# Optimization experiments

Hardware: AMD Instinct MI355X
Metric: run time of the kernel (lower is better)

The kernel has to match this reference:

```python
import jax, jax.numpy as jnp
import numpy as np

OBS_DIM, ACT_DIM, HID_DIM, FEAT = 256, 32, 1024, 512
T_STEPS, BATCH = 64, 512
LOG2PI = float(np.log(2.0 * np.pi))


def _mlp(h, w0, b0, w1, b1, w2, b2):
    # 2 hidden elu layers + linear head (MLPDecoder mean; fix_std Normal, std=1)
    x = jax.nn.elu(h @ w0.T + b0)
    x = jax.nn.elu(x @ w1.T + b1)
    return x @ w2.T + b2


def _gru(x, h, w_ih, w_hh, b_ih, b_hh):
    # torch.nn.GRUCell semantics
    gi = x @ w_ih.T + b_ih
    gh = h @ w_hh.T + b_hh
    i_r, i_z, i_n = jnp.split(gi, 3, axis=-1)
    h_r, h_z, h_n = jnp.split(gh, 3, axis=-1)
    r = jax.nn.sigmoid(i_r + h_r)
    z = jax.nn.sigmoid(i_z + h_z)
    n = jnp.tanh(i_n + r * h_n)
    return (1.0 - z) * n + z * h


def setup_inputs() -> dict:
    key = jax.random.key(0)
    ks = jax.random.split(key, 20)
    d = {}
    d['obs'] = jax.random.normal(ks[0], (T_STEPS, BATCH, OBS_DIM), jnp.float32)
    d['action'] = jax.random.normal(ks[1], (T_STEPS, BATCH, ACT_DIM), jnp.float32)
    d['reward'] = jax.random.normal(ks[2], (T_STEPS, BATCH, 1), jnp.float32)
    in_dim = OBS_DIM + ACT_DIM
    s = lambda fan_in: 1.0 / np.sqrt(fan_in)
    d['gru_w_ih'] = jax.random.normal(ks[3], (3 * HID_DIM, in_dim), jnp.float32) * s(in_dim)
    d['gru_w_hh'] = jax.random.normal(ks[4], (3 * HID_DIM, HID_DIM), jnp.float32) * s(HID_DIM)
    d['gru_b_ih'] = jnp.zeros((3 * HID_DIM,), jnp.float32)
    d['gru_b_hh'] = jnp.zeros((3 * HID_DIM,), jnp.float32)
    for name, out_dim, base in (('obs', OBS_DIM, 5), ('rew', 1, 11)):
        d[f'{name}_w0'] = jax.random.normal(ks[base], (FEAT, HID_DIM), jnp.float32) * s(HID_DIM)
        d[f'{name}_b0'] = jnp.zeros((FEAT,), jnp.float32)
        d[f'{name}_w1'] = jax.random.normal(ks[base + 1], (FEAT, FEAT), jnp.float32) * s(FEAT)
        d[f'{name}_b1'] = jnp.zeros((FEAT,), jnp.float32)
        d[f'{name}_w2'] = jax.random.normal(ks[base + 2], (out_dim, FEAT), jnp.float32) * s(FEAT)
        d[f'{name}_b2'] = jnp.zeros((out_dim,), jnp.float32)
    return d


def reference(obs, action, reward,
              gru_w_ih, gru_w_hh, gru_b_ih, gru_b_hh,
              obs_w0, obs_b0, obs_w1, obs_b1, obs_w2, obs_b2,
              rew_w0, rew_b0, rew_w1, rew_b1, rew_w2, rew_b2):
    T, B = obs.shape[0], obs.shape[1]

    def normal_logprob_sum(x, mean):
        # Normal(mean, std=1): -0.5*(x-mean)^2 - 0.5*log(2*pi), summed
        return -0.5 * jnp.sum((x - mean) ** 2 + LOG2PI)

    h0 = _gru(jnp.concatenate([obs[0], jnp.zeros_like(action[0])], axis=1),
              jnp.zeros((B, HID_DIM), obs.dtype),
              gru_w_ih, gru_w_hh, gru_b_ih, gru_b_hh)

    def step(h, xs):
        obs_t, act_t, rew_t = xs
        obs_mean = _mlp(h, obs_w0, obs_b0, obs_w1, obs_b1, obs_w2, obs_b2)
        lp_obs = normal_logprob_sum(obs_t, obs_mean)
        rew_mean = _mlp(h, rew_w0, rew_b0, rew_w1, rew_b1, rew_w2, rew_b2)
        lp_rew = normal_logprob_sum(rew_t, rew_mean)
        # feed predicted obs (mode) + ground-truth action back into the GRU
        x = jnp.concatenate([obs_mean, act_t], axis=1)
        h_next = _gru(x, h, gru_w_ih, gru_w_hh, gru_b_ih, gru_b_hh)
        return h_next, (obs_mean, rew_mean, lp_obs, lp_rew)

    _, (pre_obs, pre_reward, lp_obs, lp_rew) = jax.lax.scan(
        step, h0, (obs, action, reward))

    denom = jnp.asarray(T * B, obs.dtype)
    pre_obs_loss = -jnp.sum(lp_obs) / denom
    pre_reward_loss = -jnp.sum(lp_rew) / denom
    loss = pre_obs_loss + pre_reward_loss  # action_mimic=False -> action loss is 0
    return loss, pre_obs, pre_reward
```

## Files before the change

### kernel.cpp

```cpp
#include <hip/hip_runtime.h>
#include <stdint.h>

#define T_STEPS 64
#define BATCH   512
#define OBS_DIM 256
#define ACT_DIM 32
#define HID     1024
#define FEAT    512
#define GDIM    3072
#define KIH     288
#define NBLK    256
#define GMEMB   32
#define LOG2PI  1.8378770664093453f
#define HWREG_XCC_ID 14356

typedef __attribute__((ext_vector_type(8))) short  short8;
typedef __attribute__((ext_vector_type(4))) float  floatx4;
typedef __attribute__((ext_vector_type(4))) unsigned int uintx4;
typedef unsigned long long ull;

__device__ __forceinline__ float bf2f(unsigned int u) {
    return __uint_as_float(u << 16);
}
__device__ __forceinline__ unsigned int f2bf(float f) {
    unsigned int u = __float_as_uint(f);
    return (u + 0x7FFFu + ((u >> 16) & 1u)) >> 16;
}
__device__ __forceinline__ float elu1(float x)  { return x > 0.f ? x : expm1f(x); }
__device__ __forceinline__ float sigm(float x)  { return 1.f / (1.f + expf(-x)); }

__device__ __forceinline__ unsigned int dev_ld(const unsigned int* p) {
    return __hip_atomic_load(p, __ATOMIC_RELAXED, __HIP_MEMORY_SCOPE_AGENT);
}
__device__ __forceinline__ ull dev_ld64(const ull* p) {
    return __hip_atomic_load(p, __ATOMIC_RELAXED, __HIP_MEMORY_SCOPE_AGENT);
}
__device__ __forceinline__ void dev_st(unsigned int* p, unsigned int v) {
    __hip_atomic_store(p, v, __ATOMIC_RELAXED, __HIP_MEMORY_SCOPE_AGENT);
}
__device__ __forceinline__ float dev_ldf(const float* p) {
    return __uint_as_float(dev_ld((const unsigned int*)p));
}

template<bool COH>
__device__ __forceinline__ unsigned int a_ld(const unsigned int* p) {
    return COH ? dev_ld(p) : *p;
}
template<bool COH>
__device__ __forceinline__ ull a_ld64(const ull* p) {
    return COH ? dev_ld64(p) : *p;
}
template<bool COH>
__device__ __forceinline__ void a_st(unsigned int* p, unsigned int v) {
    if (COH) dev_st(p, v); else *p = v;
}

struct ParamsReal {
    const float* obs; const float* action; const float* reward;
    const float* b_ih; const float* b_hh;
    const float* b1o; const float* b1r; const float* b2o; const float* b2r;
    const unsigned short* Ws1; const unsigned short* Wih;
    const unsigned short* W1o; const unsigned short* W1r;
    const unsigned short* W2o; const unsigned short* w2r;
    const float* bias_s1;
    unsigned short* Z1[2]; unsigned short* Z2[2]; unsigned short* Xbuf[2];
    unsigned short* hbf[2]; unsigned short* GHb[2]; float* h[2];
    float* accum; float* out;
    int* bar;
};
#define P ParamsReal

__device__ __forceinline__ void bar_fast() {
    asm volatile("" ::: "memory");
    __builtin_amdgcn_s_barrier();
    asm volatile("" ::: "memory");
}
__device__ __forceinline__ void bar_lds() {
    asm volatile("s_waitcnt lgkmcnt(0)" ::: "memory");
    __builtin_amdgcn_s_barrier();
    asm volatile("" ::: "memory");
}

__device__ __forceinline__ void gbar(int* cnt, int* gen, int& epoch, int members) {
    __syncthreads();
    if (threadIdx.x == 0) {
        __builtin_amdgcn_fence(__ATOMIC_RELEASE, "workgroup");
        epoch++;
        int prev = __hip_atomic_fetch_add(cnt, 1, __ATOMIC_RELAXED,
                                          __HIP_MEMORY_SCOPE_AGENT);
        if (prev == members * epoch - 1) {
            __hip_atomic_store(gen, epoch, __ATOMIC_RELAXED,
                               __HIP_MEMORY_SCOPE_AGENT);
        } else {
            while (__hip_atomic_load(gen, __ATOMIC_RELAXED,
                                     __HIP_MEMORY_SCOPE_AGENT) < epoch)
                __builtin_amdgcn_s_sleep(2);
        }
        __builtin_amdgcn_fence(__ATOMIC_ACQUIRE, "workgroup");
    }
    __syncthreads();
}

template<bool COH>
__device__ __forceinline__ void s1_stage(const P& p, unsigned short* lds,
                                         int g, int m,
                                         const unsigned short* hbf_r,
                                         unsigned short* Z1_w,
                                         unsigned short* GHb_w) {
    const int tid = threadIdx.x, lane = tid & 63, wv = tid >> 6;
    const int wr = wv & 1, wc = wv >> 1, fr = lane & 15, fq = lane >> 4;
    const int rowg = g * 64, col0 = m * 128;
    unsigned short* ldsA = lds;
    unsigned short* ldsB = lds + 64 * 136;

    floatx4 acc[2][4];
    floatx4 z4 = {0.f, 0.f, 0.f, 0.f};
#pragma unroll
    for (int mi = 0; mi < 2; ++mi)
#pragma unroll
        for (int n = 0; n < 4; ++n) acc[mi][n] = z4;

    const ull* Aq = (const ull*)(hbf_r + (size_t)rowg * HID);
    const unsigned short* Bg = p.Ws1 + (size_t)col0 * HID;

    ull apf[8];
#pragma unroll
    for (int j = 0; j < 8; ++j) { int f = tid + 256 * j;
        apf[j] = a_ld64<COH>(Aq + (size_t)(f >> 5) * 256 + (f & 31)); }
    uintx4 rb0[4], rb1[4];
#pragma unroll
    for (int i = 0; i < 4; ++i) { int c = tid + 256 * i;
        const unsigned short* bp = Bg + (size_t)(c >> 3) * HID + ((c & 7) << 3);
        rb0[i] = __builtin_nontemporal_load((const uintx4*)bp);
        rb1[i] = __builtin_nontemporal_load((const uintx4*)(bp + 64)); }

#define S1_MFMA(ASUB)                                                          \
    {                                                                          \
        _Pragma("unroll")                                                      \
        for (int ks = 0; ks < 2; ++ks) {                                       \
            short8 af[2], bf8[4];                                              \
            _Pragma("unroll")                                                  \
            for (int mi = 0; mi < 2; ++mi)                                     \
                af[mi] = *(const short8*)(ldsA + (wr * 32 + mi * 16 + fr) * 136 + (ASUB) + ks * 32 + fq * 8); \
            _Pragma("unroll")                                                  \
            for (int n = 0; n < 4; ++n)                                        \
                bf8[n] = *(const short8*)(ldsB + (wc * 64 + n * 16 + fr) * 72 + ks * 32 + fq * 8); \
            _Pragma("unroll")                                                  \
            for (int mi = 0; mi < 2; ++mi)                                     \
                _Pragma("unroll")                                              \
                for (int n = 0; n < 4; ++n)                                    \
                    acc[mi][n] = __builtin_amdgcn_mfma_f32_16x16x32_bf16(      \
                        af[mi], bf8[n], acc[mi][n], 0, 0, 0);                  \
        }                                                                      \
    }

    for (int it2 = 0; it2 < 8; ++it2) {
        bar_fast();
#pragma unroll
        for (int j = 0; j < 8; ++j) { int f = tid + 256 * j;
            *(ull*)(ldsA + (size_t)(f >> 5) * 136 + ((f & 31) << 2)) = apf[j]; }
#pragma unroll
        for (int i = 0; i < 4; ++i) { int c = tid + 256 * i;
            *(uintx4*)(ldsB + (c >> 3) * 72 + ((c & 7) << 3)) = rb0[i]; }
        bar_lds();
        if (it2 < 7) {
            int c2 = it2 + 1;
#pragma unroll
            for (int j = 0; j < 8; ++j) { int f = tid + 256 * j;
                apf[j] = a_ld64<COH>(Aq + (size_t)(f >> 5) * 256 + c2 * 32 + (f & 31)); }
            int k0n = (2 * it2 + 2) * 64;
#pragma unroll
            for (int i = 0; i < 4; ++i) { int c = tid + 256 * i;
                rb0[i] = __builtin_nontemporal_load((const uintx4*)
                    (Bg + (size_t)(c >> 3) * HID + k0n + ((c & 7) << 3))); }
        }
        S1_MFMA(0);
        bar_fast();
#pragma unroll
        for (int i = 0; i < 4; ++i) { int c = tid + 256 * i;
            *(uintx4*)(ldsB + (c >> 3) * 72 + ((c & 7) << 3)) = rb1[i]; }
        bar_lds();
        if (it2 < 7) {
            int k0n = (2 * it2 + 3) * 64;
#pragma unroll
            for (int i = 0; i < 4; ++i) { int c = tid + 256 * i;
                rb1[i] = __builtin_nontemporal_load((const uintx4*)
                    (Bg + (size_t)(c >> 3) * HID + k0n + ((c & 7) << 3))); }
        }
        S1_MFMA(64);
    }
#undef S1_MFMA

    const bool isZ1 = (col0 < 1024);
#pragma unroll
    for (int mi = 0; mi < 2; ++mi)
#pragma unroll
        for (int n = 0; n < 4; ++n)
#pragma unroll
            for (int j = 0; j < 4; ++j) {
                int row = rowg + wr * 32 + mi * 16 + fq * 4 + j;
                int col = col0 + wc * 64 + n * 16 + fr;
                float v = acc[mi][n][j] + p.bias_s1[col];
                unsigned int ow = f2bf(isZ1 ? elu1(v) : v);
                unsigned int pr = __shfl_xor(ow, 1, 64);
                if (!(fr & 1)) {
                    unsigned int pk = ow | (pr << 16);
                    if (isZ1)
                        a_st<COH>((unsigned int*)(Z1_w + row * HID + col), pk);
                    else
                        a_st<COH>((unsigned int*)GHb_w + (size_t)row * 1536 + ((col - 1024) >> 1), pk);
                }
            }
}

template<bool COH>
__device__ __forceinline__ void s2_stage(const P& p, unsigned short* lds,
                                         int g, int m,
                                         const unsigned short* Z1_r,
                                         unsigned short* Z2_w) {
    const int tid = threadIdx.x, lane = tid & 63, wv = tid >> 6;
    const int wr = wv & 1, wc = wv >> 1, fr = lane & 15, fq = lane >> 4;
    const int rowg = g * 64;
    const int z = m >> 4, col0 = (m & 15) * 32;
    unsigned short* ldsA = lds;
    unsigned short* ldsB = lds + 64 * 136;

    floatx4 acc[2];
    floatx4 z4 = {0.f, 0.f, 0.f, 0.f};
    acc[0] = z4; acc[1] = z4;

    const ull* Aq = (const ull*)(Z1_r + (size_t)rowg * HID + z * FEAT);
    const unsigned short* Bg = (z ? p.W1r : p.W1o) + (size_t)col0 * FEAT;
    const float* bias = z ? p.b1r : p.b1o;

    ull apf[8];
#pragma unroll
    for (int j = 0; j < 8; ++j) { int f = tid + 256 * j;
        apf[j] = a_ld64<COH>(Aq + (size_t)(f >> 5) * 256 + (f & 31)); }
    const unsigned short* bp0 = Bg + (size_t)(tid >> 3) * FEAT + ((tid & 7) << 3);
    uintx4 rb0 = *(const uintx4*)(bp0);
    uintx4 rb1 = *(const uintx4*)(bp0 + 64);

#define S2_MFMA(ASUB)                                                          \
    {                                                                          \
        _Pragma("unroll")                                                      \
        for (int ks = 0; ks < 2; ++ks) {                                       \
            short8 bf8 = *(const short8*)(ldsB + (wc * 16 + fr) * 72 + ks * 32 + fq * 8); \
            _Pragma("unroll")                                                  \
            for (int mi = 0; mi < 2; ++mi) {                                   \
                short8 af = *(const short8*)(ldsA + (wr * 32 + mi * 16 + fr) * 136 + (ASUB) + ks * 32 + fq * 8); \
                acc[mi] = __builtin_amdgcn_mfma_f32_16x16x32_bf16(af, bf8, acc[mi], 0, 0, 0); \
            }                                                                  \
        }                                                                      \
    }

    for (int it2 = 0; it2 < 4; ++it2) {
        bar_fast();
#pragma unroll
        for (int j = 0; j < 8; ++j) { int f = tid + 256 * j;
            *(ull*)(ldsA + (size_t)(f >> 5) * 136 + ((f & 31) << 2)) = apf[j]; }
        *(uintx4*)(ldsB + (tid >> 3) * 72 + ((tid & 7) << 3)) = rb0;
        bar_lds();
        if (it2 < 3) {
            int c2 = it2 + 1;
#pragma unroll
            for (int j = 0; j < 8; ++j) { int f = tid + 256 * j;
                apf[j] = a_ld64<COH>(Aq + (size_t)(f >> 5) * 256 + c2 * 32 + (f & 31)); }
            rb0 = *(const uintx4*)(bp0 + (2 * it2 + 2) * 64);
        }
        S2_MFMA(0);
        bar_fast();
        *(uintx4*)(ldsB + (tid >> 3) * 72 + ((tid & 7) << 3)) = rb1;
        bar_lds();
        if (it2 < 3) rb1 = *(const uintx4*)(bp0 + (2 * it2 + 3) * 64);
        S2_MFMA(64);
    }
#undef S2_MFMA

#pragma unroll
    for (int mi = 0; mi < 2; ++mi)
#pragma unroll
        for (int j = 0; j < 4; ++j) {
            int row = rowg + wr * 32 + mi * 16 + fq * 4 + j;
            int col = col0 + wc * 16 + fr;
            float v = acc[mi][j] + bias[col];
            unsigned int ow = f2bf(elu1(v));
            unsigned int pr = __shfl_xor(ow, 1, 64);
            if (!(fr & 1))
                a_st<COH>((unsigned int*)(Z2_w + row * HID + z * FEAT + col), ow | (pr << 16));
        }
}

template<bool COH>
__device__ __forceinline__ void s3_stage(const P& p, unsigned short* lds,
                                         int g, int m, int t,
                                         const unsigned short* Z2_r,
                                         unsigned short* Xbuf_w) {
    const int tid = threadIdx.x, lane = tid & 63, wv = tid >> 6;
    const int wr = wv & 1, wc = wv >> 1, fr = lane & 15, fq = lane >> 4;
    const int rowg = g * 64;

    if (m < 8) {
        const int col0 = m * 32;
        unsigned short* ldsA = lds;
        unsigned short* ldsB = lds + 64 * 136;
        floatx4 acc[2];
        floatx4 z4 = {0.f, 0.f, 0.f, 0.f};
        acc[0] = z4; acc[1] = z4;

        const ull* Aq = (const ull*)(Z2_r + (size_t)rowg * HID);
        const unsigned short* Bg = p.W2o + (size_t)col0 * FEAT;

        ull apf[8];
#pragma unroll
        for (int j = 0; j < 8; ++j) { int f = tid + 256 * j;
            apf[j] = a_ld64<COH>(Aq + (size_t)(f >> 5) * 256 + (f & 31)); }
        const unsigned short* bp0 = Bg + (size_t)(tid >> 3) * FEAT + ((tid & 7) << 3);
        uintx4 rb0 = *(const uintx4*)(bp0);
        uintx4 rb1 = *(const uintx4*)(bp0 + 64);

#define S3_MFMA(ASUB)                                                          \
        {                                                                      \
            _Pragma("unroll")                                                  \
            for (int ks = 0; ks < 2; ++ks) {                                   \
                short8 bf8 = *(const short8*)(ldsB + (wc * 16 + fr) * 72 + ks * 32 + fq * 8); \
                _Pragma("unroll")                                              \
                for (int mi = 0; mi < 2; ++mi) {                               \
                    short8 af = *(const short8*)(ldsA + (wr * 32 + mi * 16 + fr) * 136 + (ASUB) + ks * 32 + fq * 8); \
                    acc[mi] = __builtin_amdgcn_mfma_f32_16x16x32_bf16(af, bf8, acc[mi], 0, 0, 0); \
                }                                                              \
            }                                                                  \
        }

        for (int it2 = 0; it2 < 4; ++it2) {
            bar_fast();
#pragma unroll
            for (int j = 0; j < 8; ++j) { int f = tid + 256 * j;
                *(ull*)(ldsA + (size_t)(f >> 5) * 136 + ((f & 31) << 2)) = apf[j]; }
            *(uintx4*)(ldsB + (tid >> 3) * 72 + ((tid & 7) << 3)) = rb0;
            bar_lds();
            if (it2 < 3) {
                int c2 = it2 + 1;
#pragma unroll
                for (int j = 0; j < 8; ++j) { int f = tid + 256 * j;
                    apf[j] = a_ld64<COH>(Aq + (size_t)(f >> 5) * 256 + c2 * 32 + (f & 31)); }
                rb0 = *(const uintx4*)(bp0 + (2 * it2 + 2) * 64);
            }
            S3_MFMA(0);
            bar_fast();
            *(uintx4*)(ldsB + (tid >> 3) * 72 + ((tid & 7) << 3)) = rb1;
            bar_lds();
            if (it2 < 3) rb1 = *(const uintx4*)(bp0 + (2 * it2 + 3) * 64);
            S3_MFMA(64);
        }
#undef S3_MFMA

        const int col = col0 + wc * 16 + fr;
        const float b2oc = p.b2o[col];
        float lsum = 0.f;
#pragma unroll
        for (int mi = 0; mi < 2; ++mi)
#pragma unroll
            for (int j = 0; j < 4; ++j) {
                int row = rowg + wr * 32 + mi * 16 + fq * 4 + j;
                float mval = acc[mi][j] + b2oc;
                size_t oidx = (size_t)t * BATCH * OBS_DIM + (size_t)row * OBS_DIM + col;
                __builtin_nontemporal_store(mval, p.out + 1 + oidx);
                unsigned int ow = f2bf(mval);
                unsigned int pr = __shfl_xor(ow, 1, 64);
                if (!(fr & 1))
                    a_st<COH>((unsigned int*)(Xbuf_w + row * KIH + col), ow | (pr << 16));
                float d = __builtin_nontemporal_load(p.obs + oidx) - mval;
                lsum += d * d;
            }
#pragma unroll
        for (int off = 32; off > 0; off >>= 1) lsum += __shfl_down(lsum, off, 64);
        if (lane == 0) atomicAdd(p.accum + 0, lsum);
    } else if (m == 8) {
        for (int e = tid; e < 64 * 16; e += 256) {
            int row = rowg + (e >> 4), cp = (e & 15) * 2;
            const float* ap = p.action + ((size_t)t * BATCH + row) * ACT_DIM + cp;
            unsigned int lo = f2bf(__builtin_nontemporal_load(ap));
            unsigned int hi = f2bf(__builtin_nontemporal_load(ap + 1));
            a_st<COH>((unsigned int*)(Xbuf_w + row * KIH + OBS_DIM + cp), lo | (hi << 16));
        }
    } else if (m >= 16) {
        const int row = rowg + (m - 16) * 4 + wv;
        const ull* zq = (const ull*)(Z2_r + (size_t)row * HID + FEAT) + lane * 2;
        ull z0 = a_ld64<COH>(zq);
        ull z1 = a_ld64<COH>(zq + 1);
        short8 w8 = *(const short8*)(p.w2r + lane * 8);
        float s = 0.f;
#pragma unroll
        for (int k = 0; k < 4; ++k) {
            unsigned int u = (unsigned int)(z0 >> (16 * k)) & 0xFFFFu;
            s += bf2f(u) * bf2f((unsigned int)(unsigned short)w8[k]);
        }
#pragma unroll
        for (int k = 0; k < 4; ++k) {
            unsigned int u = (unsigned int)(z1 >> (16 * k)) & 0xFFFFu;
            s += bf2f(u) * bf2f((unsigned int)(unsigned short)w8[4 + k]);
        }
#pragma unroll
        for (int off = 32; off > 0; off >>= 1) s += __shfl_down(s, off, 64);
        if (lane == 0) {
            float mm = s + p.b2r[0];
            __builtin_nontemporal_store(
                mm, p.out + 1 + (size_t)T_STEPS * BATCH * OBS_DIM + (size_t)t * BATCH + row);
            float d = __builtin_nontemporal_load(p.reward + (size_t)t * BATCH + row) - mm;
            atomicAdd(p.accum + 1, d * d);
        }
    }
}

template<bool COH>
__device__ __forceinline__ void s4_stage(const P& p, unsigned short* lds,
                                         int g, int m, int use_gh,
                                         const unsigned short* Xbuf_r,
                                         const unsigned short* GHb_r,
                                         const float* h_r,
                                         float* h_w, unsigned short* hbf_w) {
    const int tid = threadIdx.x, lane = tid & 63, wv = tid >> 6;
    const int wr = wv & 1, wc = wv >> 1, fr = lane & 15, fq = lane >> 4;
    const int rowg = g * 64;
    const int col0 = m * 32;
    unsigned short* ldsA = lds;
    unsigned short* ldsB = lds + 64 * 104;

    floatx4 acc[3][2];
    floatx4 z4 = {0.f, 0.f, 0.f, 0.f};
#pragma unroll
    for (int g3 = 0; g3 < 3; ++g3) { acc[g3][0] = z4; acc[g3][1] = z4; }

    const ull* Xq = (const ull*)(Xbuf_r + (size_t)rowg * KIH);
    ull apf[6];
#pragma unroll
    for (int j = 0; j < 6; ++j) { int f = tid + 256 * j;
        apf[j] = a_ld64<COH>(Xq + (size_t)(f / 24) * 72 + (f % 24)); }

    uintx4 wpfA[5], wpfB[5];
#pragma unroll
    for (int j = 0; j < 5; ++j) { int f = tid + 256 * j;
        if (f < 1152) { int r = f / 12, ko = (f - r * 12) * 8;
            const unsigned short* wp =
                p.Wih + (size_t)((r >> 5) * HID + col0 + (r & 31)) * KIH + ko;
            wpfA[j] = __builtin_nontemporal_load((const uintx4*)wp);
            wpfB[j] = __builtin_nontemporal_load((const uintx4*)(wp + 96)); } }

#pragma unroll
    for (int c = 0; c < 3; ++c) {
        bar_fast();
#pragma unroll
        for (int j = 0; j < 6; ++j) { int f = tid + 256 * j;
            *(ull*)(ldsA + (size_t)(f / 24) * 104 + ((f % 24) << 2)) = apf[j]; }
#pragma unroll
        for (int j = 0; j < 5; ++j) { int f = tid + 256 * j;
            if (f < 1152) { int r = f / 12, ko = (f - r * 12) * 8;
                *(uintx4*)(ldsB + r * 104 + ko) = (c & 1) ? wpfB[j] : wpfA[j]; } }
        bar_lds();
        if (c < 2) {
#pragma unroll
            for (int j = 0; j < 6; ++j) { int f = tid + 256 * j;
                apf[j] = a_ld64<COH>(Xq + (size_t)(f / 24) * 72 + (c + 1) * 24 + (f % 24)); }
        }
        if (c == 0) {
#pragma unroll
            for (int j = 0; j < 5; ++j) { int f = tid + 256 * j;
                if (f < 1152) { int r = f / 12, ko = (f - r * 12) * 8;
                    wpfA[j] = __builtin_nontemporal_load((const uintx4*)
                        (p.Wih + (size_t)((r >> 5) * HID + col0 + (r & 31)) * KIH + 192 + ko)); } }
        }
#pragma unroll
        for (int ks = 0; ks < 3; ++ks) {
            short8 af[2];
#pragma unroll
            for (int mi = 0; mi < 2; ++mi)
                af[mi] = *(const short8*)(ldsA + (wr * 32 + mi * 16 + fr) * 104 + ks * 32 + fq * 8);
#pragma unroll
            for (int g3 = 0; g3 < 3; ++g3) {
                short8 bf8 = *(const short8*)(ldsB + (g3 * 32 + wc * 16 + fr) * 104 + ks * 32 + fq * 8);
#pragma unroll
                for (int mi = 0; mi < 2; ++mi)
                    acc[g3][mi] = __builtin_amdgcn_mfma_f32_16x16x32_bf16(
                        af[mi], bf8, acc[g3][mi], 0, 0, 0);
            }
        }
    }

    const int col = col0 + wc * 16 + fr;
    const float bir = p.b_ih[col];
    const float biz = p.b_ih[HID + col];
    const float bin = p.b_ih[2 * HID + col];
    float hrv[2][4], hzv[2][4], hnv[2][4], hpv[2][4];
    if (use_gh) {
        const unsigned int* GW = (const unsigned int*)GHb_r;
        const int cw = col >> 1, hi = col & 1;
#pragma unroll
        for (int mi = 0; mi < 2; ++mi)
#pragma unroll
            for (int j = 0; j < 4; ++j) {
                int row = rowg + wr * 32 + mi * 16 + fq * 4 + j;
                unsigned int ur = a_ld<COH>(GW + (size_t)row * 1536 + cw);
                unsigned int uz = a_ld<COH>(GW + (size_t)row * 1536 + 512 + cw);
                unsigned int un = a_ld<COH>(GW + (size_t)row * 1536 + 1024 + cw);
                hrv[mi][j] = bf2f(hi ? (ur >> 16) : (ur & 0xFFFFu));
                hzv[mi][j] = bf2f(hi ? (uz >> 16) : (uz & 0xFFFFu));
                hnv[mi][j] = bf2f(hi ? (un >> 16) : (un & 0xFFFFu));
                hpv[mi][j] = __uint_as_float(a_ld<COH>((const unsigned int*)(h_r + (size_t)row * HID + col)));
            }
    } else {
        float br = p.b_hh[col], bz = p.b_hh[HID + col], bn = p.b_hh[2 * HID + col];
#pragma unroll
        for (int mi = 0; mi < 2; ++mi)
#pragma unroll
            for (int j = 0; j < 4; ++j) {
                hrv[mi][j] = br; hzv[mi][j] = bz; hnv[mi][j] = bn; hpv[mi][j] = 0.f;
            }
    }
#pragma unroll
    for (int mi = 0; mi < 2; ++mi)
#pragma unroll
        for (int j = 0; j < 4; ++j) {
            int row = rowg + wr * 32 + mi * 16 + fq * 4 + j;
            float r  = sigm(acc[0][mi][j] + bir + hrv[mi][j]);
            float z  = sigm(acc[1][mi][j] + biz + hzv[mi][j]);
            float nn = tanhf(acc[2][mi][j] + bin + r * hnv[mi][j]);
            float hv = (1.f - z) * nn + z * hpv[mi][j];
            a_st<COH>((unsigned int*)(h_w + (size_t)row * HID + col), __float_as_uint(hv));
            unsigned int ow = f2bf(hv);
            unsigned int pr = __shfl_xor(ow, 1, 64);
            if (!(fr & 1))
                a_st<COH>((unsigned int*)(hbf_w + row * HID + col), ow | (pr << 16));
        }
}

template<bool COH>
__device__ void rollout(const P& p, unsigned short* lds, int g, int m) {
    int* gcnt = p.bar + g * 128;
    int* ggen = p.bar + g * 128 + 64;
    int epoch = 0;

    s4_stage<COH>(p, lds, g, m, 0, p.Xbuf[1], p.GHb[0], p.h[0], p.h[0], p.hbf[0]);
    gbar(gcnt, ggen, epoch, GMEMB);

    for (int t = 0; t < T_STEPS; ++t) {
        const int pr = t & 1, nx = (t + 1) & 1;
        s1_stage<COH>(p, lds, g, m, p.hbf[pr], p.Z1[pr], p.GHb[pr]);
        gbar(gcnt, ggen, epoch, GMEMB);
        s2_stage<COH>(p, lds, g, m, p.Z1[pr], p.Z2[pr]);
        gbar(gcnt, ggen, epoch, GMEMB);
        s3_stage<COH>(p, lds, g, m, t, p.Z2[pr], p.Xbuf[pr]);
        gbar(gcnt, ggen, epoch, GMEMB);
        if (t < T_STEPS - 1) {
            s4_stage<COH>(p, lds, g, m, 1, p.Xbuf[pr], p.GHb[pr], p.h[pr],
                          p.h[nx], p.hbf[nx]);
            gbar(gcnt, ggen, epoch, GMEMB);
        }
    }
}

__global__ __launch_bounds__(256, 1) void k_persist(P p) {
    __shared__ unsigned short lds[17920];
    __shared__ int sh[3];

    const int bid = blockIdx.x;
    if (threadIdx.x == 0) {
        unsigned int xcd = __builtin_amdgcn_s_getreg(HWREG_XCC_ID) & 7u;
        int r = __hip_atomic_fetch_add(p.bar + 1024 + xcd, 1,
                                       __ATOMIC_RELAXED, __HIP_MEMORY_SCOPE_AGENT);
        sh[0] = (int)xcd; sh[1] = r;
    }
    int repoch = 0;
    gbar(p.bar + 1200, p.bar + 1264, repoch, NBLK);
    if (threadIdx.x == 0) {
        int ok = (sh[1] < 32);
        for (int i = 0; i < 8; ++i)
            ok &= (dev_ld((const unsigned int*)(p.bar + 1024 + i)) == 32u);
        sh[2] = ok;
    }
    __syncthreads();

    if (sh[2]) rollout<false>(p, lds, sh[0], sh[1]);
    else       rollout<true >(p, lds, bid & 7, bid >> 3);

    gbar(p.bar + 1200, p.bar + 1264, repoch, NBLK);
    if (bid == 0 && threadIdx.x == 0) {
        const float inv = 1.f / (float)(T_STEPS * BATCH);
        float a0 = dev_ldf(p.accum + 0);
        float a1 = dev_ldf(p.accum + 1);
        p.out[0] = 0.5f * a0 * inv + 128.f * LOG2PI
                 + 0.5f * a1 * inv + 0.5f * LOG2PI;
    }
}

__global__ void k_convert(
    const float* __restrict__ ow0, const float* __restrict__ rw0,
    const float* __restrict__ whh, const float* __restrict__ wih,
    const float* __restrict__ ow1, const float* __restrict__ rw1,
    const float* __restrict__ ow2, const float* __restrict__ rw2,
    const float* __restrict__ ob0, const float* __restrict__ rb0,
    const float* __restrict__ bhh,
    unsigned short* __restrict__ Ws1, unsigned short* __restrict__ Wih,
    unsigned short* __restrict__ W1o, unsigned short* __restrict__ W1r,
    unsigned short* __restrict__ W2o, unsigned short* __restrict__ w2r,
    float* __restrict__ bias_s1)
{
    const int i0 = blockIdx.x * 256 + threadIdx.x;
    const int stride = gridDim.x * 256;
    for (int i = i0; i < 4096 * 1024; i += stride) {
        int row = i >> 10;
        float v = (row < 512) ? ow0[i]
                : (row < 1024) ? rw0[i - 512 * 1024]
                               : whh[i - 1024 * 1024];
        Ws1[i] = (unsigned short)f2bf(v);
    }
    for (int i = i0; i < GDIM * KIH; i += stride) Wih[i] = (unsigned short)f2bf(wih[i]);
    for (int i = i0; i < FEAT * FEAT; i += stride) {
        W1o[i] = (unsigned short)f2bf(ow1[i]);
        W1r[i] = (unsigned short)f2bf(rw1[i]);
    }
    for (int i = i0; i < OBS_DIM * FEAT; i += stride) W2o[i] = (unsigned short)f2bf(ow2[i]);
    for (int i = i0; i < FEAT; i += stride) w2r[i] = (unsigned short)f2bf(rw2[i]);
    for (int i = i0; i < 4096; i += stride)
        bias_s1[i] = (i < 512) ? ob0[i] : (i < 1024) ? rb0[i - 512] : bhh[i - 1024];
}

__global__ void k_init(const float* __restrict__ obs,
                       unsigned short* __restrict__ Xbuf1,
                       float* __restrict__ accum,
                       int* __restrict__ bar)
{
    int i = blockIdx.x * 256 + threadIdx.x;
    if (i < BATCH * KIH) {
        int row = i / KIH, col = i - row * KIH;
        Xbuf1[i] = (col < OBS_DIM) ? (unsigned short)f2bf(obs[row * OBS_DIM + col])
                                   : (unsigned short)0;
    }
    if (i < 2)    accum[i] = 0.f;
    if (i < 1536) bar[i] = 0;
}

extern "C" void kernel_launch(void* const* d_in, const int* in_sizes, int n_in,
                              void* d_out, int out_size, void* d_ws, size_t ws_size,
                              hipStream_t stream)
{
    const float* obs      = (const float*)d_in[0];
    const float* action   = (const float*)d_in[1];
    const float* reward   = (const float*)d_in[2];
    const float* gru_w_ih = (const float*)d_in[3];
    const float* gru_w_hh = (const float*)d_in[4];
    const float* gru_b_ih = (const float*)d_in[5];
    const float* gru_b_hh = (const float*)d_in[6];
    const float* obs_w0   = (const float*)d_in[7];
    const float* obs_b0   = (const float*)d_in[8];
    const float* obs_w1   = (const float*)d_in[9];
    const float* obs_b1   = (const float*)d_in[10];
    const float* obs_w2   = (const float*)d_in[11];
    const float* obs_b2   = (const float*)d_in[12];
    const float* rew_w0   = (const float*)d_in[13];
    const float* rew_b0   = (const float*)d_in[14];
    const float* rew_w1   = (const float*)d_in[15];
    const float* rew_b1   = (const float*)d_in[16];
    const float* rew_w2   = (const float*)d_in[17];
    const float* rew_b2   = (const float*)d_in[18];

    char* ws = (char*)d_ws;
    auto alloc = [&](size_t bytes) -> char* {
        char* pr = ws;
        ws += (bytes + 255) & ~(size_t)255;
        return pr;
    };
    unsigned short* Ws1  = (unsigned short*)alloc((size_t)4096 * 1024 * 2);
    unsigned short* Wih  = (unsigned short*)alloc((size_t)GDIM * KIH * 2);
    unsigned short* W1o  = (unsigned short*)alloc((size_t)FEAT * FEAT * 2);
    unsigned short* W1r  = (unsigned short*)alloc((size_t)FEAT * FEAT * 2);
    unsigned short* W2o  = (unsigned short*)alloc((size_t)OBS_DIM * FEAT * 2);
    unsigned short* w2r  = (unsigned short*)alloc((size_t)FEAT * 2);
    float* bias_s1       = (float*)alloc((size_t)4096 * 4);
    unsigned short* Z1a  = (unsigned short*)alloc((size_t)BATCH * HID * 2);
    unsigned short* Z1b  = (unsigned short*)alloc((size_t)BATCH * HID * 2);
    unsigned short* Z2a  = (unsigned short*)alloc((size_t)BATCH * HID * 2);
    unsigned short* Z2b  = (unsigned short*)alloc((size_t)BATCH * HID * 2);
    unsigned short* GHa  = (unsigned short*)alloc((size_t)BATCH * GDIM * 2);
    unsigned short* GHbB = (unsigned short*)alloc((size_t)BATCH * GDIM * 2);
    unsigned short* Xba  = (unsigned short*)alloc((size_t)BATCH * KIH * 2);
    unsigned short* Xbb  = (unsigned short*)alloc((size_t)BATCH * KIH * 2);
    float* ha            = (float*)alloc((size_t)BATCH * HID * 4);
    float* hb            = (float*)alloc((size_t)BATCH * HID * 4);
    unsigned short* hfa  = (unsigned short*)alloc((size_t)BATCH * HID * 2);
    unsigned short* hfb  = (unsigned short*)alloc((size_t)BATCH * HID * 2);
    float* accum         = (float*)alloc(256);
    int*   bar           = (int*)alloc(8192);

    dim3 blk(256);

    k_convert<<<dim3(1024), blk, 0, stream>>>(
        obs_w0, rew_w0, gru_w_hh, gru_w_ih, obs_w1, rew_w1, obs_w2, rew_w2,
        obs_b0, rew_b0, gru_b_hh, Ws1, Wih, W1o, W1r, W2o, w2r, bias_s1);

    k_init<<<dim3((BATCH * KIH + 255) / 256), blk, 0, stream>>>(obs, Xbb, accum, bar);

    P hp;
    hp.obs = obs; hp.action = action; hp.reward = reward;
    hp.b_ih = gru_b_ih; hp.b_hh = gru_b_hh;
    hp.b1o = obs_b1; hp.b1r = rew_b1; hp.b2o = obs_b2; hp.b2r = rew_b2;
    hp.Ws1 = Ws1; hp.Wih = Wih; hp.W1o = W1o; hp.W1r = W1r;
    hp.W2o = W2o; hp.w2r = w2r; hp.bias_s1 = bias_s1;
    hp.Z1[0] = Z1a; hp.Z1[1] = Z1b;
    hp.Z2[0] = Z2a; hp.Z2[1] = Z2b;
    hp.Xbuf[0] = Xba; hp.Xbuf[1] = Xbb;
    hp.hbf[0] = hfa; hp.hbf[1] = hfb;
    hp.GHb[0] = GHa; hp.GHb[1] = GHbB;
    hp.h[0] = ha; hp.h[1] = hb;
    hp.accum = accum; hp.out = (float*)d_out;
    hp.bar = bar;

    k_persist<<<dim3(NBLK), blk, 0, stream>>>(hp);
}
```

Before: 2.542 ms.

## Double-buffer LDS in GEMM stages and replace counter barrier with per-block flags

The s1/s2/s3 GEMM loops now use two LDS buffers with four register prefetch slots and a 64-wide K step. This drops one of the two barriers per K step and keeps more global loads in flight. The group barrier changes from a single atomic counter plus generation word to per-block epoch flags. Each block writes its own flag and 32 lanes poll all members' flags, which avoids contention on one atomic. In exchange it uses more LDS, more registers and a larger barrier area, and more threads spin-poll.

```diff
diff --git a/kernel.cpp b/kernel.cpp
--- a/kernel.cpp
+++ b/kernel.cpp
@@ -101,6 +101,22 @@
     __syncthreads();
 }
 
+__device__ __forceinline__ void gbar_flags(int* fbase, int m, int& epoch) {
+    __syncthreads();
+    epoch++;
+    if (threadIdx.x == 0) {
+        __builtin_amdgcn_fence(__ATOMIC_RELEASE, "workgroup");
+        dev_st((unsigned int*)(fbase + m * 16), (unsigned int)epoch);
+    }
+    if (threadIdx.x < 64) {
+        const unsigned int* fp =
+            (const unsigned int*)(fbase + (threadIdx.x & 31) * 16);
+        while ((int)dev_ld(fp) < epoch) __builtin_amdgcn_s_sleep(4);
+        __builtin_amdgcn_fence(__ATOMIC_ACQUIRE, "workgroup");
+    }
+    __syncthreads();
+}
+
 template<bool COH>
 __device__ __forceinline__ void s1_stage(const P& p, unsigned short* lds,
                                          int g, int m,
@@ -110,8 +126,8 @@
     const int tid = threadIdx.x, lane = tid & 63, wv = tid >> 6;
     const int wr = wv & 1, wc = wv >> 1, fr = lane & 15, fq = lane >> 4;
     const int rowg = g * 64, col0 = m * 128;
-    unsigned short* ldsA = lds;
-    unsigned short* ldsB = lds + 64 * 136;
+    unsigned short* b0 = lds;
+    unsigned short* b1 = lds + 13568;
 
     floatx4 acc[2][4];
     floatx4 z4 = {0.f, 0.f, 0.f, 0.f};
@@ -123,72 +139,57 @@
     const ull* Aq = (const ull*)(hbf_r + (size_t)rowg * HID);
     const unsigned short* Bg = p.Ws1 + (size_t)col0 * HID;
 
-    ull apf[8];
-#pragma unroll
-    for (int j = 0; j < 8; ++j) { int f = tid + 256 * j;
-        apf[j] = a_ld64<COH>(Aq + (size_t)(f >> 5) * 256 + (f & 31)); }
-    uintx4 rb0[4], rb1[4];
-#pragma unroll
-    for (int i = 0; i < 4; ++i) { int c = tid + 256 * i;
-        const unsigned short* bp = Bg + (size_t)(c >> 3) * HID + ((c & 7) << 3);
-        rb0[i] = __builtin_nontemporal_load((const uintx4*)bp);
-        rb1[i] = __builtin_nontemporal_load((const uintx4*)(bp + 64)); }
-
-#define S1_MFMA(ASUB)                                                          \
-    {                                                                          \
-        _Pragma("unroll")                                                      \
-        for (int ks = 0; ks < 2; ++ks) {                                       \
-            short8 af[2], bf8[4];                                              \
-            _Pragma("unroll")                                                  \
-            for (int mi = 0; mi < 2; ++mi)                                     \
-                af[mi] = *(const short8*)(ldsA + (wr * 32 + mi * 16 + fr) * 136 + (ASUB) + ks * 32 + fq * 8); \
-            _Pragma("unroll")                                                  \
-            for (int n = 0; n < 4; ++n)                                        \
-                bf8[n] = *(const short8*)(ldsB + (wc * 64 + n * 16 + fr) * 72 + ks * 32 + fq * 8); \
-            _Pragma("unroll")                                                  \
-            for (int mi = 0; mi < 2; ++mi)                                     \
-                _Pragma("unroll")                                              \
-                for (int n = 0; n < 4; ++n)                                    \
-                    acc[mi][n] = __builtin_amdgcn_mfma_f32_16x16x32_bf16(      \
-                        af[mi], bf8[n], acc[mi][n], 0, 0, 0);                  \
-        }                                                                      \
-    }
-
-    for (int it2 = 0; it2 < 8; ++it2) {
-        bar_fast();
-#pragma unroll
-        for (int j = 0; j < 8; ++j) { int f = tid + 256 * j;
-            *(ull*)(ldsA + (size_t)(f >> 5) * 136 + ((f & 31) << 2)) = apf[j]; }
-#pragma unroll
-        for (int i = 0; i < 4; ++i) { int c = tid + 256 * i;
-            *(uintx4*)(ldsB + (c >> 3) * 72 + ((c & 7) << 3)) = rb0[i]; }
-        bar_lds();
-        if (it2 < 7) {
-            int c2 = it2 + 1;
-#pragma unroll
-            for (int j = 0; j < 8; ++j) { int f = tid + 256 * j;
-                apf[j] = a_ld64<COH>(Aq + (size_t)(f >> 5) * 256 + c2 * 32 + (f & 31)); }
-            int k0n = (2 * it2 + 2) * 64;
-#pragma unroll
-            for (int i = 0; i < 4; ++i) { int c = tid + 256 * i;
-                rb0[i] = __builtin_nontemporal_load((const uintx4*)
-                    (Bg + (size_t)(c >> 3) * HID + k0n + ((c & 7) << 3))); }
-        }
-        S1_MFMA(0);
-        bar_fast();
-#pragma unroll
-        for (int i = 0; i < 4; ++i) { int c = tid + 256 * i;
-            *(uintx4*)(ldsB + (c >> 3) * 72 + ((c & 7) << 3)) = rb1[i]; }
-        bar_lds();
-        if (it2 < 7) {
-            int k0n = (2 * it2 + 3) * 64;
-#pragma unroll
-            for (int i = 0; i < 4; ++i) { int c = tid + 256 * i;
-                rb1[i] = __builtin_nontemporal_load((const uintx4*)
-                    (Bg + (size_t)(c >> 3) * HID + k0n + ((c & 7) << 3))); }
-        }
-        S1_MFMA(64);
-    }
+    ull a0[4], a1[4], a2[4], a3[4];
+    uintx4 rb0[4], rb1[4], rb2[4], rb3[4];
+
+#define S1_LDA(reg, s)                                                         \
+    { _Pragma("unroll") for (int j = 0; j < 4; ++j) { int f = tid + 256 * j;   \
+        reg[j] = a_ld64<COH>(Aq + (size_t)(f >> 4) * 256 + (s) * 16 + (f & 15)); } }
+#define S1_LDB(reg, s)                                                         \
+    { _Pragma("unroll") for (int i = 0; i < 4; ++i) { int c = tid + 256 * i;   \
+        reg[i] = __builtin_nontemporal_load((const uintx4*)                    \
+            (Bg + (size_t)(c >> 3) * HID + (s) * 64 + ((c & 7) << 3))); } }
+#define S1_STAGE(BUF, breg, areg)                                              \
+    { unsigned short* A_ = (BUF); unsigned short* B_ = (BUF) + 4352;           \
+      _Pragma("unroll") for (int j = 0; j < 4; ++j) { int f = tid + 256 * j;   \
+        *(ull*)(A_ + (f >> 4) * 68 + ((f & 15) << 2)) = areg[j]; }             \
+      _Pragma("unroll") for (int i = 0; i < 4; ++i) { int c = tid + 256 * i;   \
+        *(uintx4*)(B_ + (c >> 3) * 72 + ((c & 7) << 3)) = breg[i]; } }
+#define S1_MFMA(BUF)                                                           \
+    { unsigned short* A_ = (BUF); unsigned short* B_ = (BUF) + 4352;           \
+      _Pragma("unroll") for (int ks = 0; ks < 2; ++ks) {                       \
+        short8 af[2], bf8[4];                                                  \
+        _Pragma("unroll") for (int mi = 0; mi < 2; ++mi)                       \
+            af[mi] = *(const short8*)(A_ + (wr * 32 + mi * 16 + fr) * 68 + ks * 32 + fq * 8); \
+        _Pragma("unroll") for (int n = 0; n < 4; ++n)                          \
+            bf8[n] = *(const short8*)(B_ + (wc * 64 + n * 16 + fr) * 72 + ks * 32 + fq * 8);  \
+        _Pragma("unroll") for (int mi = 0; mi < 2; ++mi)                       \
+            _Pragma("unroll") for (int n = 0; n < 4; ++n)                      \
+                acc[mi][n] = __builtin_amdgcn_mfma_f32_16x16x32_bf16(          \
+                    af[mi], bf8[n], acc[mi][n], 0, 0, 0); } }
+
+    S1_LDA(a0, 0); S1_LDA(a1, 1); S1_LDA(a2, 2); S1_LDA(a3, 3);
+    S1_LDB(rb0, 0); S1_LDB(rb1, 1); S1_LDB(rb2, 2); S1_LDB(rb3, 3);
+
+#pragma unroll 1
+    for (int it4 = 0; it4 < 4; ++it4) {
+        const int s = it4 * 4;
+        S1_STAGE(b0, rb0, a0); bar_lds();
+        if (s + 4 < 16) { S1_LDB(rb0, s + 4); S1_LDA(a0, s + 4); }
+        S1_MFMA(b0);
+        S1_STAGE(b1, rb1, a1); bar_lds();
+        if (s + 5 < 16) { S1_LDB(rb1, s + 5); S1_LDA(a1, s + 5); }
+        S1_MFMA(b1);
+        S1_STAGE(b0, rb2, a2); bar_lds();
+        if (s + 6 < 16) { S1_LDB(rb2, s + 6); S1_LDA(a2, s + 6); }
+        S1_MFMA(b0);
+        S1_STAGE(b1, rb3, a3); bar_lds();
+        if (s + 7 < 16) { S1_LDB(rb3, s + 7); S1_LDA(a3, s + 7); }
+        S1_MFMA(b1);
+    }
+#undef S1_LDA
+#undef S1_LDB
+#undef S1_STAGE
 #undef S1_MFMA
 
     const bool isZ1 = (col0 < 1024);
@@ -214,16 +215,21 @@
 }
 
 template<bool COH>
+__device__ __forceinline__ void s2s3_gemm(const unsigned short* lds_unused,
+                                          int dummy) {}
+
+template<bool COH>
 __device__ __forceinline__ void s2_stage(const P& p, unsigned short* lds,
                                          int g, int m,
                                          const unsigned short* Z1_r,
                                          unsigned short* Z2_w) {
     const int tid = threadIdx.x, lane = tid & 63, wv = tid >> 6;
-    const int wr = wv & 1, wc = wv >> 1, fr = lane & 15, fq = lane >> 4;
+    const int wr = wv & 1, wc = wv >> 1;
+    const int fr = lane & 15, fq = lane >> 4;
     const int rowg = g * 64;
     const int z = m >> 4, col0 = (m & 15) * 32;
-    unsigned short* ldsA = lds;
-    unsigned short* ldsB = lds + 64 * 136;
+    unsigned short* b0 = lds;
+    unsigned short* b1 = lds + 6656;
 
     floatx4 acc[2];
     floatx4 z4 = {0.f, 0.f, 0.f, 0.f};
@@ -233,48 +239,49 @@
     const unsigned short* Bg = (z ? p.W1r : p.W1o) + (size_t)col0 * FEAT;
     const float* bias = z ? p.b1r : p.b1o;
 
-    ull apf[8];
-#pragma unroll
-    for (int j = 0; j < 8; ++j) { int f = tid + 256 * j;
-        apf[j] = a_ld64<COH>(Aq + (size_t)(f >> 5) * 256 + (f & 31)); }
-    const unsigned short* bp0 = Bg + (size_t)(tid >> 3) * FEAT + ((tid & 7) << 3);
-    uintx4 rb0 = *(const uintx4*)(bp0);
-    uintx4 rb1 = *(const uintx4*)(bp0 + 64);
-
-#define S2_MFMA(ASUB)                                                          \
-    {                                                                          \
-        _Pragma("unroll")                                                      \
-        for (int ks = 0; ks < 2; ++ks) {                                       \
-            short8 bf8 = *(const short8*)(ldsB + (wc * 16 + fr) * 72 + ks * 32 + fq * 8); \
-            _Pragma("unroll")                                                  \
-            for (int mi = 0; mi < 2; ++mi) {                                   \
-                short8 af = *(const short8*)(ldsA + (wr * 32 + mi * 16 + fr) * 136 + (ASUB) + ks * 32 + fq * 8); \
-                acc[mi] = __builtin_amdgcn_mfma_f32_16x16x32_bf16(af, bf8, acc[mi], 0, 0, 0); \
-            }                                                                  \
-        }                                                                      \
-    }
-
-    for (int it2 = 0; it2 < 4; ++it2) {
-        bar_fast();
-#pragma unroll
-        for (int j = 0; j < 8; ++j) { int f = tid + 256 * j;
-            *(ull*)(ldsA + (size_t)(f >> 5) * 136 + ((f & 31) << 2)) = apf[j]; }
-        *(uintx4*)(ldsB + (tid >> 3) * 72 + ((tid & 7) << 3)) = rb0;
-        bar_lds();
-        if (it2 < 3) {
-            int c2 = it2 + 1;
-#pragma unroll
-            for (int j = 0; j < 8; ++j) { int f = tid + 256 * j;
-                apf[j] = a_ld64<COH>(Aq + (size_t)(f >> 5) * 256 + c2 * 32 + (f & 31)); }
-            rb0 = *(const uintx4*)(bp0 + (2 * it2 + 2) * 64);
-        }
-        S2_MFMA(0);
-        bar_fast();
-        *(uintx4*)(ldsB + (tid >> 3) * 72 + ((tid & 7) << 3)) = rb1;
-        bar_lds();
-        if (it2 < 3) rb1 = *(const uintx4*)(bp0 + (2 * it2 + 3) * 64);
-        S2_MFMA(64);
-    }
+    ull a0[4], a1[4], a2[4], a3[4];
+    uintx4 rb0, rb1, rb2, rb3;
+
+#define S2_LDA(reg, s)                                                         \
+    { _Pragma("unroll") for (int j = 0; j < 4; ++j) { int f = tid + 256 * j;   \
+        reg[j] = a_ld64<COH>(Aq + (size_t)(f >> 4) * 256 + (s) * 16 + (f & 15)); } }
+#define S2_LDB(reg, s)                                                         \
+    { reg = *(const uintx4*)(Bg + (size_t)(tid >> 3) * FEAT + (s) * 64 + ((tid & 7) << 3)); }
+#define S2_STAGE(BUF, breg, areg)                                              \
+    { unsigned short* A_ = (BUF); unsigned short* B_ = (BUF) + 4352;           \
+      _Pragma("unroll") for (int j = 0; j < 4; ++j) { int f = tid + 256 * j;   \
+        *(ull*)(A_ + (f >> 4) * 68 + ((f & 15) << 2)) = areg[j]; }             \
+      *(uintx4*)(B_ + (tid >> 3) * 72 + ((tid & 7) << 3)) = breg; }
+#define S2_MFMA(BUF)                                                           \
+    { unsigned short* A_ = (BUF); unsigned short* B_ = (BUF) + 4352;           \
+      _Pragma("unroll") for (int ks = 0; ks < 2; ++ks) {                       \
+        short8 bf8 = *(const short8*)(B_ + (wc * 16 + fr) * 72 + ks * 32 + fq * 8); \
+        _Pragma("unroll") for (int mi = 0; mi < 2; ++mi) {                     \
+            short8 af = *(const short8*)(A_ + (wr * 32 + mi * 16 + fr) * 68 + ks * 32 + fq * 8); \
+            acc[mi] = __builtin_amdgcn_mfma_f32_16x16x32_bf16(af, bf8, acc[mi], 0, 0, 0); } } }
+
+    S2_LDA(a0, 0); S2_LDA(a1, 1); S2_LDA(a2, 2); S2_LDA(a3, 3);
+    S2_LDB(rb0, 0); S2_LDB(rb1, 1); S2_LDB(rb2, 2); S2_LDB(rb3, 3);
+
+#pragma unroll 1
+    for (int it4 = 0; it4 < 2; ++it4) {
+        const int s = it4 * 4;
+        S2_STAGE(b0, rb0, a0); bar_lds();
+        if (s + 4 < 8) { S2_LDB(rb0, s + 4); S2_LDA(a0, s + 4); }
+        S2_MFMA(b0);
+        S2_STAGE(b1, rb1, a1); bar_lds();
+        if (s + 5 < 8) { S2_LDB(rb1, s + 5); S2_LDA(a1, s + 5); }
+        S2_MFMA(b1);
+        S2_STAGE(b0, rb2, a2); bar_lds();
+        if (s + 6 < 8) { S2_LDB(rb2, s + 6); S2_LDA(a2, s + 6); }
+        S2_MFMA(b0);
+        S2_STAGE(b1, rb3, a3); bar_lds();
+        if (s + 7 < 8) { S2_LDB(rb3, s + 7); S2_LDA(a3, s + 7); }
+        S2_MFMA(b1);
+    }
+#undef S2_LDA
+#undef S2_LDB
+#undef S2_STAGE
 #undef S2_MFMA
 
 #pragma unroll
@@ -297,13 +304,14 @@
                                          const unsigned short* Z2_r,
                                          unsigned short* Xbuf_w) {
     const int tid = threadIdx.x, lane = tid & 63, wv = tid >> 6;
-    const int wr = wv & 1, wc = wv >> 1, fr = lane & 15, fq = lane >> 4;
+    const int wr = wv & 1, wc = wv >> 1;
+    const int fr = lane & 15, fq = lane >> 4;
     const int rowg = g * 64;
 
     if (m < 8) {
         const int col0 = m * 32;
-        unsigned short* ldsA = lds;
-        unsigned short* ldsB = lds + 64 * 136;
+        unsigned short* b0 = lds;
+        unsigned short* b1 = lds + 6656;
         floatx4 acc[2];
         floatx4 z4 = {0.f, 0.f, 0.f, 0.f};
         acc[0] = z4; acc[1] = z4;
@@ -311,48 +319,49 @@
         const ull* Aq = (const ull*)(Z2_r + (size_t)rowg * HID);
         const unsigned short* Bg = p.W2o + (size_t)col0 * FEAT;
 
-        ull apf[8];
-#pragma unroll
-        for (int j = 0; j < 8; ++j) { int f = tid + 256 * j;
-            apf[j] = a_ld64<COH>(Aq + (size_t)(f >> 5) * 256 + (f & 31)); }
-        const unsigned short* bp0 = Bg + (size_t)(tid >> 3) * FEAT + ((tid & 7) << 3);
-        uintx4 rb0 = *(const uintx4*)(bp0);
-        uintx4 rb1 = *(const uintx4*)(bp0 + 64);
-
-#define S3_MFMA(ASUB)                                                          \
-        {                                                                      \
-            _Pragma("unroll")                                                  \
-            for (int ks = 0; ks < 2; ++ks) {                                   \
-                short8 bf8 = *(const short8*)(ldsB + (wc * 16 + fr) * 72 + ks * 32 + fq * 8); \
-                _Pragma("unroll")                                              \
-                for (int mi = 0; mi < 2; ++mi) {                               \
-                    short8 af = *(const short8*)(ldsA + (wr * 32 + mi * 16 + fr) * 136 + (ASUB) + ks * 32 + fq * 8); \
-                    acc[mi] = __builtin_amdgcn_mfma_f32_16x16x32_bf16(af, bf8, acc[mi], 0, 0, 0); \
-                }                                                              \
-            }                                                                  \
-        }
-
-        for (int it2 = 0; it2 < 4; ++it2) {
-            bar_fast();
-#pragma unroll
-            for (int j = 0; j < 8; ++j) { int f = tid + 256 * j;
-                *(ull*)(ldsA + (size_t)(f >> 5) * 136 + ((f & 31) << 2)) = apf[j]; }
-            *(uintx4*)(ldsB + (tid >> 3) * 72 + ((tid & 7) << 3)) = rb0;
-            bar_lds();
-            if (it2 < 3) {
-                int c2 = it2 + 1;
-#pragma unroll
-                for (int j = 0; j < 8; ++j) { int f = tid + 256 * j;
-                    apf[j] = a_ld64<COH>(Aq + (size_t)(f >> 5) * 256 + c2 * 32 + (f & 31)); }
-                rb0 = *(const uintx4*)(bp0 + (2 * it2 + 2) * 64);
-            }
-            S3_MFMA(0);
-            bar_fast();
-            *(uintx4*)(ldsB + (tid >> 3) * 72 + ((tid & 7) << 3)) = rb1;
-            bar_lds();
-            if (it2 < 3) rb1 = *(const uintx4*)(bp0 + (2 * it2 + 3) * 64);
-            S3_MFMA(64);
-        }
+        ull a0[4], a1[4], a2[4], a3[4];
+        uintx4 rb0, rb1, rb2, rb3;
+
+#define S3_LDA(reg, s)                                                         \
+    { _Pragma("unroll") for (int j = 0; j < 4; ++j) { int f = tid + 256 * j;   \
+        reg[j] = a_ld64<COH>(Aq + (size_t)(f >> 4) * 256 + (s) * 16 + (f & 15)); } }
+#define S3_LDB(reg, s)                                                         \
+    { reg = *(const uintx4*)(Bg + (size_t)(tid >> 3) * FEAT + (s) * 64 + ((tid & 7) << 3)); }
+#define S3_STAGE(BUF, breg, areg)                                              \
+    { unsigned short* A_ = (BUF); unsigned short* B_ = (BUF) + 4352;           \
+      _Pragma("unroll") for (int j = 0; j < 4; ++j) { int f = tid + 256 * j;   \
+        *(ull*)(A_ + (f >> 4) * 68 + ((f & 15) << 2)) = areg[j]; }             \
+      *(uintx4*)(B_ + (tid >> 3) * 72 + ((tid & 7) << 3)) = breg; }
+#define S3_MFMA(BUF)                                                           \
+    { unsigned short* A_ = (BUF); unsigned short* B_ = (BUF) + 4352;           \
+      _Pragma("unroll") for (int ks = 0; ks < 2; ++ks) {                       \
+        short8 bf8 = *(const short8*)(B_ + (wc * 16 + fr) * 72 + ks * 32 + fq * 8); \
+        _Pragma("unroll") for (int mi = 0; mi < 2; ++mi) {                     \
+            short8 af = *(const short8*)(A_ + (wr * 32 + mi * 16 + fr) * 68 + ks * 32 + fq * 8); \
+            acc[mi] = __builtin_amdgcn_mfma_f32_16x16x32_bf16(af, bf8, acc[mi], 0, 0, 0); } } }
+
+        S3_LDA(a0, 0); S3_LDA(a1, 1); S3_LDA(a2, 2); S3_LDA(a3, 3);
+        S3_LDB(rb0, 0); S3_LDB(rb1, 1); S3_LDB(rb2, 2); S3_LDB(rb3, 3);
+
+#pragma unroll 1
+        for (int it4 = 0; it4 < 2; ++it4) {
+            const int s = it4 * 4;
+            S3_STAGE(b0, rb0, a0); bar_lds();
+            if (s + 4 < 8) { S3_LDB(rb0, s + 4); S3_LDA(a0, s + 4); }
+            S3_MFMA(b0);
+            S3_STAGE(b1, rb1, a1); bar_lds();
+            if (s + 5 < 8) { S3_LDB(rb1, s + 5); S3_LDA(a1, s + 5); }
+            S3_MFMA(b1);
+            S3_STAGE(b0, rb2, a2); bar_lds();
+            if (s + 6 < 8) { S3_LDB(rb2, s + 6); S3_LDA(a2, s + 6); }
+            S3_MFMA(b0);
+            S3_STAGE(b1, rb3, a3); bar_lds();
+            if (s + 7 < 8) { S3_LDB(rb3, s + 7); S3_LDA(a3, s + 7); }
+            S3_MFMA(b1);
+        }
+#undef S3_LDA
+#undef S3_LDB
+#undef S3_STAGE
 #undef S3_MFMA
 
         const int col = col0 + wc * 16 + fr;
@@ -421,7 +430,8 @@
                                          const float* h_r,
                                          float* h_w, unsigned short* hbf_w) {
     const int tid = threadIdx.x, lane = tid & 63, wv = tid >> 6;
-    const int wr = wv & 1, wc = wv >> 1, fr = lane & 15, fq = lane >> 4;
+    const int wr = wv & 1, wc = wv >> 1;
+    const int fr = lane & 15, fq = lane >> 4;
     const int rowg = g * 64;
     const int col0 = m * 32;
     unsigned short* ldsA = lds;
@@ -536,31 +546,30 @@
 
 template<bool COH>
 __device__ void rollout(const P& p, unsigned short* lds, int g, int m) {
-    int* gcnt = p.bar + g * 128;
-    int* ggen = p.bar + g * 128 + 64;
-    int epoch = 0;
+    int* fbase = p.bar + 2048 + g * 512;
+    int fep = 0;
 
     s4_stage<COH>(p, lds, g, m, 0, p.Xbuf[1], p.GHb[0], p.h[0], p.h[0], p.hbf[0]);
-    gbar(gcnt, ggen, epoch, GMEMB);
+    gbar_flags(fbase, m, fep);
 
     for (int t = 0; t < T_STEPS; ++t) {
         const int pr = t & 1, nx = (t + 1) & 1;
         s1_stage<COH>(p, lds, g, m, p.hbf[pr], p.Z1[pr], p.GHb[pr]);
-        gbar(gcnt, ggen, epoch, GMEMB);
+        gbar_flags(fbase, m, fep);
         s2_stage<COH>(p, lds, g, m, p.Z1[pr], p.Z2[pr]);
-        gbar(gcnt, ggen, epoch, GMEMB);
+        gbar_flags(fbase, m, fep);
         s3_stage<COH>(p, lds, g, m, t, p.Z2[pr], p.Xbuf[pr]);
-        gbar(gcnt, ggen, epoch, GMEMB);
+        gbar_flags(fbase, m, fep);
         if (t < T_STEPS - 1) {
             s4_stage<COH>(p, lds, g, m, 1, p.Xbuf[pr], p.GHb[pr], p.h[pr],
                           p.h[nx], p.hbf[nx]);
-            gbar(gcnt, ggen, epoch, GMEMB);
+            gbar_flags(fbase, m, fep);
         }
     }
 }
 
 __global__ __launch_bounds__(256, 1) void k_persist(P p) {
-    __shared__ unsigned short lds[17920];
+    __shared__ unsigned short lds[27136];
     __shared__ int sh[3];
 
     const int bid = blockIdx.x;
@@ -637,7 +646,7 @@
                                    : (unsigned short)0;
     }
     if (i < 2)    accum[i] = 0.f;
-    if (i < 1536) bar[i] = 0;
+    if (i < 8192) bar[i] = 0;
 }
 
 extern "C" void kernel_launch(void* const* d_in, const int* in_sizes, int n_in,
@@ -690,15 +699,13 @@
     unsigned short* hfa  = (unsigned short*)alloc((size_t)BATCH * HID * 2);
     unsigned short* hfb  = (unsigned short*)alloc((size_t)BATCH * HID * 2);
     float* accum         = (float*)alloc(256);
-    int*   bar           = (int*)alloc(8192);
-
-    dim3 blk(256);
-
-    k_convert<<<dim3(1024), blk, 0, stream>>>(
+    int*   bar           = (int*)alloc(32768);
+
+    k_convert<<<dim3(1024), dim3(256), 0, stream>>>(
         obs_w0, rew_w0, gru_w_hh, gru_w_ih, obs_w1, rew_w1, obs_w2, rew_w2,
         obs_b0, rew_b0, gru_b_hh, Ws1, Wih, W1o, W1r, W2o, w2r, bias_s1);
 
-    k_init<<<dim3((BATCH * KIH + 255) / 256), blk, 0, stream>>>(obs, Xbb, accum, bar);
+    k_init<<<dim3((BATCH * KIH + 255) / 256), dim3(256), 0, stream>>>(obs, Xbb, accum, bar);
 
     P hp;
     hp.obs = obs; hp.action = action; hp.reward = reward;
@@ -715,5 +722,5 @@
     hp.accum = accum; hp.out = (float*)d_out;
     hp.bar = bar;
 
-    k_persist<<<dim3(NBLK), blk, 0, stream>>>(hp);
-}
+    k_persist<<<dim3(NBLK), dim3(256), 0, stream>>>(hp);
+}
```

New measurement: 3.111 ms. 1.22x slower.
